# Optimization experiments

Measured on AMD Instinct MI355X. Metric: run time of the kernel, lower is better.

Reference implementation:

```python
import jax, jax.numpy as jnp
import numpy as np

B, L, D, C = 4, 512, 128, 128
EPS = 1e-7  # Keras backend epsilon


def setup_inputs() -> dict:
    key = jax.random.key(0)
    ks = jax.random.split(key, 4)
    inps = jax.random.normal(ks[0], (B, L, D), dtype=jnp.float32)
    # glorot_normal-ish scale for weights
    wei_t = jax.random.normal(ks[1], (D, C), dtype=jnp.float32) * (2.0 / (D + C)) ** 0.5
    wei_x = jax.random.normal(ks[2], (D, C), dtype=jnp.float32) * (2.0 / (D + C)) ** 0.5
    bxh = jnp.zeros((C,), dtype=jnp.float32)
    wei_a = jax.random.normal(ks[3], (C,), dtype=jnp.float32) * (2.0 / (C + 1)) ** 0.5
    bxa = jnp.zeros((), dtype=jnp.float32)
    return {"inps": inps, "wei_t": wei_t, "wei_x": wei_x, "bxh": bxh,
            "wei_a": wei_a, "bxa": bxa}


def reference(inps, wei_t, wei_x, bxh, wei_a, bxa):
    # Additive (Bahdanau-style) pairwise self-attention, no mask.
    qt = inps @ wei_t                      # [B, L, C] (query-side projection)
    kx = inps @ wei_x                      # [B, L, C] (key-side projection)
    # Pairwise hidden: [B, L, L, C]
    h = jnp.tanh(qt[:, :, None, :] + kx[:, None, :, :] + bxh)
    scores = jnp.einsum('bijc,c->bij', h, wei_a) + bxa  # [B, L, L]
    # activation_func=None -> linear (identity)
    e = jnp.exp(scores - jnp.max(scores, axis=-1, keepdims=True))
    a = e / (jnp.sum(e, axis=-1, keepdims=True) + EPS)   # [B, L, L]
    out = jnp.einsum('bij,bjd->bid', a, inps)            # [B, L, D]
    return out
```

## Files before the change

kernel.cpp:

```cpp
#include <hip/hip_runtime.h>

#define NB 4
#define SL 512
#define DD 128
#define CC 128

__device__ __forceinline__ float fexp2(float x) { return __builtin_amdgcn_exp2f(x); }
__device__ __forceinline__ float frcp(float x)  { return __builtin_amdgcn_rcpf(x); }

__global__ __launch_bounds__(256) void proj_kernel(
    const float* __restrict__ inps, const float* __restrict__ wei_t,
    const float* __restrict__ wei_x, const float* __restrict__ bxh,
    float* __restrict__ E, float* __restrict__ F)
{
    const float K2 = 2.8853900817779268f;
    const int row0 = blockIdx.x * 2;
    const int b    = row0 >> 9;
    const int i0   = row0 & 511;
    const int c    = threadIdx.x & 127;
    const int sel  = threadIdx.x >> 7;

    const float* W  = sel ? wei_x : wei_t;
    const float* r0 = inps + (size_t)row0 * DD;
    const float* r1 = r0 + DD;

    float a0 = 0.f, a1 = 0.f;
    #pragma unroll 8
    for (int k = 0; k < DD; ++k) {
        float w = W[k * CC + c];
        a0 = fmaf(r0[k], w, a0);
        a1 = fmaf(r1[k], w, a1);
    }

    if (sel == 0) {
        float bb = bxh[c];
        E[(size_t)(row0 + 0) * CC + c] = fexp2(K2 * (a0 + bb));
        E[(size_t)(row0 + 1) * CC + c] = fexp2(K2 * (a1 + bb));
    } else {
        float2 v = {fexp2(K2 * a0), fexp2(K2 * a1)};
        *reinterpret_cast<float2*>(&F[((size_t)b * CC + c) * SL + i0]) = v;
    }
}

__global__ __launch_bounds__(512, 4) void attn_kernel(
    const float* __restrict__ inps, const float* __restrict__ wei_a,
    const float* __restrict__ E, const float* __restrict__ F,
    float* __restrict__ out)
{
    __shared__ float4 upk[CC];
    __shared__ float smrg[256 * 9];
    __shared__ float scT[SL * 4];
    __shared__ float redw[4 * 4];
    __shared__ float redbuf[4 * 16 * DD];

    const int blk = blockIdx.x;
    const int b   = blk >> 7;
    const int i0  = (blk & 127) * 4;
    const int bi0 = b * SL + i0;
    const int tid = threadIdx.x;
    const int jt  = tid & 255;
    const int ch  = tid >> 8;
    const int j0  = jt * 2;

    if (tid < CC) {
        float4 u;
        u.x = E[(size_t)(bi0 + 0) * CC + tid];
        u.y = E[(size_t)(bi0 + 1) * CC + tid];
        u.z = E[(size_t)(bi0 + 2) * CC + tid];
        u.w = E[(size_t)(bi0 + 3) * CC + tid];
        upk[tid] = u;
    }
    __syncthreads();

    const int c0 = ch * 64;
    const float* fb = F + ((size_t)b * CC + c0) * SL + j0;
    const float4* up = upk + c0;
    const float* wa = wei_a + c0;
    float sx[4] = {0.f, 0.f, 0.f, 0.f};
    float sy[4] = {0.f, 0.f, 0.f, 0.f};
    #pragma unroll 4
    for (int cp = 0; cp < 32; ++cp) {
        float2 f0 = *reinterpret_cast<const float2*>(&fb[(size_t)(2 * cp) * SL]);
        float2 f1 = *reinterpret_cast<const float2*>(&fb[(size_t)(2 * cp + 1) * SL]);
        float4 u0 = up[2 * cp];
        float4 u1 = up[2 * cp + 1];
        float wa0 = wa[2 * cp], wa1 = wa[2 * cp + 1];
        const float* u0p = reinterpret_cast<const float*>(&u0);
        const float* u1p = reinterpret_cast<const float*>(&u1);
        #pragma unroll
        for (int i = 0; i < 4; ++i) {
            float ax = fmaf(u0p[i], f0.x, 1.0f);
            float bx = fmaf(u1p[i], f1.x, 1.0f);
            float numx = fmaf(wa0, bx, wa1 * ax);
            sx[i] = fmaf(numx, frcp(ax * bx), sx[i]);
            float ay = fmaf(u0p[i], f0.y, 1.0f);
            float by = fmaf(u1p[i], f1.y, 1.0f);
            float numy = fmaf(wa0, by, wa1 * ay);
            sy[i] = fmaf(numy, frcp(ay * by), sy[i]);
        }
    }

    if (ch == 1) {
        #pragma unroll
        for (int i = 0; i < 4; ++i) {
            smrg[jt * 9 + i]     = sx[i];
            smrg[jt * 9 + 4 + i] = sy[i];
        }
    }
    __syncthreads();

    if (ch == 0) {
        const float KE = -2.8853900817779268f;
        float ex[4], ey[4];
        const int lane = tid & 63, wv = tid >> 6;
        #pragma unroll
        for (int i = 0; i < 4; ++i) {
            float si = sx[i] + smrg[jt * 9 + i];
            float ti = sy[i] + smrg[jt * 9 + 4 + i];
            ex[i] = fexp2(si * KE);
            ey[i] = fexp2(ti * KE);
            float t = ex[i] + ey[i];
            #pragma unroll
            for (int off = 32; off > 0; off >>= 1)
                t += __shfl_xor(t, off, 64);
            if (lane == 0) redw[i * 4 + wv] = t;
        }
        __syncthreads();
        float4 av0, av1;
        {
            float S0 = redw[0] + redw[1] + redw[2] + redw[3];
            float S1 = redw[4] + redw[5] + redw[6] + redw[7];
            float S2 = redw[8] + redw[9] + redw[10] + redw[11];
            float S3 = redw[12] + redw[13] + redw[14] + redw[15];
            float r0 = frcp(S0 + 1e-7f), r1 = frcp(S1 + 1e-7f);
            float r2 = frcp(S2 + 1e-7f), r3 = frcp(S3 + 1e-7f);
            av0 = make_float4(ex[0] * r0, ex[1] * r1, ex[2] * r2, ex[3] * r3);
            av1 = make_float4(ey[0] * r0, ey[1] * r1, ey[2] * r2, ey[3] * r3);
        }
        *reinterpret_cast<float4*>(&scT[j0 * 4])     = av0;
        *reinterpret_cast<float4*>(&scT[j0 * 4 + 4]) = av1;
    } else {
        __syncthreads();
    }
    __syncthreads();

    const int dq = (tid & 31) * 4;
    const int jq = tid >> 5;
    const float* ibase = inps + (size_t)b * SL * DD;
    float4 acc0 = {0,0,0,0}, acc1 = {0,0,0,0}, acc2 = {0,0,0,0}, acc3 = {0,0,0,0};
    const int jb = jq * 32;
    #pragma unroll 4
    for (int jj = 0; jj < 32; ++jj) {
        int jx = jb + jj;
        float4 v  = *reinterpret_cast<const float4*>(ibase + (size_t)jx * DD + dq);
        float4 a4 = *reinterpret_cast<const float4*>(&scT[jx * 4]);
        acc0.x = fmaf(a4.x, v.x, acc0.x); acc0.y = fmaf(a4.x, v.y, acc0.y);
        acc0.z = fmaf(a4.x, v.z, acc0.z); acc0.w = fmaf(a4.x, v.w, acc0.w);
        acc1.x = fmaf(a4.y, v.x, acc1.x); acc1.y = fmaf(a4.y, v.y, acc1.y);
        acc1.z = fmaf(a4.y, v.z, acc1.z); acc1.w = fmaf(a4.y, v.w, acc1.w);
        acc2.x = fmaf(a4.z, v.x, acc2.x); acc2.y = fmaf(a4.z, v.y, acc2.y);
        acc2.z = fmaf(a4.z, v.z, acc2.z); acc2.w = fmaf(a4.z, v.w, acc2.w);
        acc3.x = fmaf(a4.w, v.x, acc3.x); acc3.y = fmaf(a4.w, v.y, acc3.y);
        acc3.z = fmaf(a4.w, v.z, acc3.z); acc3.w = fmaf(a4.w, v.w, acc3.w);
    }
    *reinterpret_cast<float4*>(&redbuf[(0 * 16 + jq) * DD + dq]) = acc0;
    *reinterpret_cast<float4*>(&redbuf[(1 * 16 + jq) * DD + dq]) = acc1;
    *reinterpret_cast<float4*>(&redbuf[(2 * 16 + jq) * DD + dq]) = acc2;
    *reinterpret_cast<float4*>(&redbuf[(3 * 16 + jq) * DD + dq]) = acc3;
    __syncthreads();
    {
        int i = tid >> 7, d = tid & 127;
        float sum = 0.f;
        #pragma unroll
        for (int q = 0; q < 16; ++q) sum += redbuf[(i * 16 + q) * DD + d];
        out[(size_t)(bi0 + i) * DD + d] = sum;
    }
}

extern "C" void kernel_launch(void* const* d_in, const int* in_sizes, int n_in,
                              void* d_out, int out_size, void* d_ws, size_t ws_size,
                              hipStream_t stream) {
    const float* inps  = (const float*)d_in[0];
    const float* wei_t = (const float*)d_in[1];
    const float* wei_x = (const float*)d_in[2];
    const float* bxh   = (const float*)d_in[3];
    const float* wei_a = (const float*)d_in[4];
    float* out = (float*)d_out;

    float* E = (float*)d_ws;
    float* F = E + (size_t)NB * SL * CC;

    proj_kernel<<<NB * SL / 2, 256, 0, stream>>>(inps, wei_t, wei_x, bxh, E, F);
    attn_kernel<<<NB * SL / 4, 512, 0, stream>>>(inps, wei_a, E, F, out);
}
```

Measured before the change: 91.01 us.

## Split attention score channel loop across four thread groups with 1024-thread blocks

Doubles the attention block to 1024 threads so the channel reduction over C is split into four 32-channel quarters instead of two 64-channel halves, merging partials through a shared pool buffer. The score buffer is aliased with the output reduction buffer to keep LDS usage down. Only half the threads do the weighted-sum phase. The aim is more parallelism in the dominant pairwise tanh/score phase, at the cost of a larger merge step and higher per-block register pressure under the new launch bounds.

```diff
diff --git a/kernel.cpp b/kernel.cpp
--- a/kernel.cpp
+++ b/kernel.cpp
@@ -42,16 +42,15 @@
     }
 }
 
-__global__ __launch_bounds__(512, 4) void attn_kernel(
+__global__ __launch_bounds__(1024, 8) void attn_kernel(
     const float* __restrict__ inps, const float* __restrict__ wei_a,
     const float* __restrict__ E, const float* __restrict__ F,
     float* __restrict__ out)
 {
     __shared__ float4 upk[CC];
-    __shared__ float smrg[256 * 9];
+    __shared__ float pool[4 * 16 * DD];
     __shared__ float scT[SL * 4];
     __shared__ float redw[4 * 4];
-    __shared__ float redbuf[4 * 16 * DD];
 
     const int blk = blockIdx.x;
     const int b   = blk >> 7;
@@ -59,7 +58,7 @@
     const int bi0 = b * SL + i0;
     const int tid = threadIdx.x;
     const int jt  = tid & 255;
-    const int ch  = tid >> 8;
+    const int cq  = tid >> 8;
     const int j0  = jt * 2;
 
     if (tid < CC) {
@@ -72,14 +71,14 @@
     }
     __syncthreads();
 
-    const int c0 = ch * 64;
+    const int c0 = cq * 32;
     const float* fb = F + ((size_t)b * CC + c0) * SL + j0;
     const float4* up = upk + c0;
     const float* wa = wei_a + c0;
     float sx[4] = {0.f, 0.f, 0.f, 0.f};
     float sy[4] = {0.f, 0.f, 0.f, 0.f};
     #pragma unroll 4
-    for (int cp = 0; cp < 32; ++cp) {
+    for (int cp = 0; cp < 16; ++cp) {
         float2 f0 = *reinterpret_cast<const float2*>(&fb[(size_t)(2 * cp) * SL]);
         float2 f1 = *reinterpret_cast<const float2*>(&fb[(size_t)(2 * cp + 1) * SL]);
         float4 u0 = up[2 * cp];
@@ -100,25 +99,27 @@
         }
     }
 
-    if (ch == 1) {
+    if (cq > 0) {
+        float* m = &pool[(cq - 1) * 2304 + jt * 9];
         #pragma unroll
-        for (int i = 0; i < 4; ++i) {
-            smrg[jt * 9 + i]     = sx[i];
-            smrg[jt * 9 + 4 + i] = sy[i];
-        }
+        for (int i = 0; i < 4; ++i) { m[i] = sx[i]; m[4 + i] = sy[i]; }
     }
     __syncthreads();
 
-    if (ch == 0) {
+    if (cq == 0) {
+        #pragma unroll
+        for (int seg = 0; seg < 3; ++seg) {
+            const float* m = &pool[seg * 2304 + jt * 9];
+            #pragma unroll
+            for (int i = 0; i < 4; ++i) { sx[i] += m[i]; sy[i] += m[4 + i]; }
+        }
         const float KE = -2.8853900817779268f;
         float ex[4], ey[4];
         const int lane = tid & 63, wv = tid >> 6;
         #pragma unroll
         for (int i = 0; i < 4; ++i) {
-            float si = sx[i] + smrg[jt * 9 + i];
-            float ti = sy[i] + smrg[jt * 9 + 4 + i];
-            ex[i] = fexp2(si * KE);
-            ey[i] = fexp2(ti * KE);
+            ex[i] = fexp2(sx[i] * KE);
+            ey[i] = fexp2(sy[i] * KE);
             float t = ex[i] + ey[i];
             #pragma unroll
             for (int off = 32; off > 0; off >>= 1)
@@ -144,35 +145,37 @@
     }
     __syncthreads();
 
-    const int dq = (tid & 31) * 4;
-    const int jq = tid >> 5;
-    const float* ibase = inps + (size_t)b * SL * DD;
-    float4 acc0 = {0,0,0,0}, acc1 = {0,0,0,0}, acc2 = {0,0,0,0}, acc3 = {0,0,0,0};
-    const int jb = jq * 32;
-    #pragma unroll 4
-    for (int jj = 0; jj < 32; ++jj) {
-        int jx = jb + jj;
-        float4 v  = *reinterpret_cast<const float4*>(ibase + (size_t)jx * DD + dq);
-        float4 a4 = *reinterpret_cast<const float4*>(&scT[jx * 4]);
-        acc0.x = fmaf(a4.x, v.x, acc0.x); acc0.y = fmaf(a4.x, v.y, acc0.y);
-        acc0.z = fmaf(a4.x, v.z, acc0.z); acc0.w = fmaf(a4.x, v.w, acc0.w);
-        acc1.x = fmaf(a4.y, v.x, acc1.x); acc1.y = fmaf(a4.y, v.y, acc1.y);
-        acc1.z = fmaf(a4.y, v.z, acc1.z); acc1.w = fmaf(a4.y, v.w, acc1.w);
-        acc2.x = fmaf(a4.z, v.x, acc2.x); acc2.y = fmaf(a4.z, v.y, acc2.y);
-        acc2.z = fmaf(a4.z, v.z, acc2.z); acc2.w = fmaf(a4.z, v.w, acc2.w);
-        acc3.x = fmaf(a4.w, v.x, acc3.x); acc3.y = fmaf(a4.w, v.y, acc3.y);
-        acc3.z = fmaf(a4.w, v.z, acc3.z); acc3.w = fmaf(a4.w, v.w, acc3.w);
+    if (tid < 512) {
+        const int dq = (tid & 31) * 4;
+        const int jq = tid >> 5;
+        const float* ibase = inps + (size_t)b * SL * DD;
+        float4 acc0 = {0,0,0,0}, acc1 = {0,0,0,0}, acc2 = {0,0,0,0}, acc3 = {0,0,0,0};
+        const int jb = jq * 32;
+        #pragma unroll 4
+        for (int jj = 0; jj < 32; ++jj) {
+            int jx = jb + jj;
+            float4 v  = *reinterpret_cast<const float4*>(ibase + (size_t)jx * DD + dq);
+            float4 a4 = *reinterpret_cast<const float4*>(&scT[jx * 4]);
+            acc0.x = fmaf(a4.x, v.x, acc0.x); acc0.y = fmaf(a4.x, v.y, acc0.y);
+            acc0.z = fmaf(a4.x, v.z, acc0.z); acc0.w = fmaf(a4.x, v.w, acc0.w);
+            acc1.x = fmaf(a4.y, v.x, acc1.x); acc1.y = fmaf(a4.y, v.y, acc1.y);
+            acc1.z = fmaf(a4.y, v.z, acc1.z); acc1.w = fmaf(a4.y, v.w, acc1.w);
+            acc2.x = fmaf(a4.z, v.x, acc2.x); acc2.y = fmaf(a4.z, v.y, acc2.y);
+            acc2.z = fmaf(a4.z, v.z, acc2.z); acc2.w = fmaf(a4.z, v.w, acc2.w);
+            acc3.x = fmaf(a4.w, v.x, acc3.x); acc3.y = fmaf(a4.w, v.y, acc3.y);
+            acc3.z = fmaf(a4.w, v.z, acc3.z); acc3.w = fmaf(a4.w, v.w, acc3.w);
+        }
+        *reinterpret_cast<float4*>(&pool[(0 * 16 + jq) * DD + dq]) = acc0;
+        *reinterpret_cast<float4*>(&pool[(1 * 16 + jq) * DD + dq]) = acc1;
+        *reinterpret_cast<float4*>(&pool[(2 * 16 + jq) * DD + dq]) = acc2;
+        *reinterpret_cast<float4*>(&pool[(3 * 16 + jq) * DD + dq]) = acc3;
     }
-    *reinterpret_cast<float4*>(&redbuf[(0 * 16 + jq) * DD + dq]) = acc0;
-    *reinterpret_cast<float4*>(&redbuf[(1 * 16 + jq) * DD + dq]) = acc1;
-    *reinterpret_cast<float4*>(&redbuf[(2 * 16 + jq) * DD + dq]) = acc2;
-    *reinterpret_cast<float4*>(&redbuf[(3 * 16 + jq) * DD + dq]) = acc3;
     __syncthreads();
-    {
+    if (tid < 512) {
         int i = tid >> 7, d = tid & 127;
         float sum = 0.f;
         #pragma unroll
-        for (int q = 0; q < 16; ++q) sum += redbuf[(i * 16 + q) * DD + d];
+        for (int q = 0; q < 16; ++q) sum += pool[(i * 16 + q) * DD + d];
         out[(size_t)(bi0 + i) * DD + d] = sum;
     }
 }
@@ -191,5 +194,5 @@
     float* F = E + (size_t)NB * SL * CC;
 
     proj_kernel<<<NB * SL / 2, 256, 0, stream>>>(inps, wei_t, wei_x, bxh, E, F);
-    attn_kernel<<<NB * SL / 4, 512, 0, stream>>>(inps, wei_a, E, F, out);
+    attn_kernel<<<NB * SL / 4, 1024, 0, stream>>>(inps, wei_a, E, F, out);
 }
```

Result: no change. 90.21 us (-0.9%).
